# Kernel tuning notes

Measured on AMD Instinct MI355X. Metric: run time of the kernel, lower is better.

The kernel has to match this reference:

```python
import jax, jax.numpy as jnp
import numpy as np

SLIDING_WINDOW = 512  # matches init kwarg
BLOCK_STRIDE = 32     # tokens per cache page


def setup_inputs() -> dict:
    key = jax.random.key(0)
    k0, k1, k2, k3 = jax.random.split(key, 4)
    B, S, HQ, HKV, D = 2, 2048, 32, 8, 128
    nb = S // BLOCK_STRIDE
    q = jax.random.normal(k0, (B, S, HQ, D), jnp.float32)
    k = jax.random.normal(k1, (B, S, HKV, D), jnp.float32)
    v = jax.random.normal(k2, (B, S, HKV, D), jnp.float32)
    sink = jax.random.normal(k3, (HQ,), jnp.float32)
    cache_state = jnp.zeros((B * nb, 2, HKV, BLOCK_STRIDE, D), jnp.float32)
    seq_block_ids = jnp.arange(B * nb, dtype=jnp.int32).reshape(B, nb)
    return {"q": q, "k": k, "v": v, "cache_state": cache_state,
            "seq_block_ids": seq_block_ids, "sink": sink}


def reference(q, k, v, cache_state, seq_block_ids, sink):
    B, S, HQ, D = q.shape
    HKV = k.shape[2]
    G = HQ // HKV  # GQA group size
    stride = cache_state.shape[3]
    nb = S // stride

    # --- write prefill K/V into the paged cache ---
    # pages laid out [num_pages, k/v, HKV, stride, D]
    k_pg = k.reshape(B, nb, stride, HKV, D).transpose(0, 1, 3, 2, 4).reshape(B * nb, HKV, stride, D)
    v_pg = v.reshape(B, nb, stride, HKV, D).transpose(0, 1, 3, 2, 4).reshape(B * nb, HKV, stride, D)
    ids = seq_block_ids.reshape(-1)
    new_cache = cache_state.at[ids, 0].set(k_pg).at[ids, 1].set(v_pg)

    # --- sliding-window causal attention with sink logits (GQA, no repeat) ---
    scale = 1.0 / np.sqrt(D).astype(np.float32)
    qg = q.reshape(B, S, HKV, G, D)
    # scores: [B, HKV, G, Sq, Sk]
    scores = jnp.einsum('bqhgd,bshd->bhgqs', qg, k) * scale
    i = jnp.arange(S)[:, None]
    j = jnp.arange(S)[None, :]
    allowed = (j <= i) & ((i - j) < SLIDING_WINDOW)  # causal banded mask
    neg = jnp.finfo(scores.dtype).min
    scores = jnp.where(allowed, scores, neg)
    # per-head sink logit appended as extra key column, dropped after softmax
    sink_col = jnp.broadcast_to(sink.reshape(HKV, G)[None, :, :, None, None], (B, HKV, G, S, 1))
    probs = jax.nn.softmax(jnp.concatenate([scores, sink_col], axis=-1), axis=-1)[..., :S]
    out = jnp.einsum('bhgqs,bshd->bqhgd', probs, v).reshape(B, S, HQ, D)
    return out, new_cache
```

## Files before the change

kernel.cpp:

```cpp
#include <hip/hip_runtime.h>
#include <hip/hip_bf16.h>
#include <stdint.h>

#define BB 2
#define SS 2048
#define HQ 32
#define HKV 8
#define DD 128
#define WIN 512

typedef __bf16 bf16x8 __attribute__((ext_vector_type(8)));
typedef float f32x16 __attribute__((ext_vector_type(16)));

__device__ __forceinline__ bf16x8 cvt8(float4 a, float4 b, float s) {
  bf16x8 r;
  r[0] = (__bf16)(a.x * s); r[1] = (__bf16)(a.y * s);
  r[2] = (__bf16)(a.z * s); r[3] = (__bf16)(a.w * s);
  r[4] = (__bf16)(b.x * s); r[5] = (__bf16)(b.y * s);
  r[6] = (__bf16)(b.z * s); r[7] = (__bf16)(b.w * s);
  return r;
}

__device__ __forceinline__ uint32_t pk2(float lo, float hi) {
  uint32_t w;
  asm("v_cvt_pk_bf16_f32 %0, %1, %2" : "=v"(w) : "v"(lo), "v"(hi));
  return w;
}

__device__ __forceinline__ unsigned short bfu(float x) {
  union { __bf16 b; unsigned short u; } c; c.b = (__bf16)x; return c.u;
}

#define SWZ(r) ((((r) ^ ((r) >> 3)) & 7) << 4)

__global__ __launch_bounds__(512, 2) void attn_kernel(
    const float* __restrict__ qg, const float* __restrict__ sinkg,
    float* __restrict__ outg,
    const unsigned short* __restrict__ kbg, const unsigned short* __restrict__ vtg)
{
  const int col = (blockIdx.x & 7) + 8 * ((blockIdx.x >> 3) & 1);
  const int rank = blockIdx.x >> 4;
  const int qtile = rank < 24 ? rank + 8 : 31 - rank;
  const int hkv = col & 7, b = col >> 3;
  const int qb = qtile * 64;
  const int tid = threadIdx.x;
  const int wave = tid >> 6, lane = tid & 63;
  const int c5 = lane & 31, hi = lane >> 5;
  const int hq = (hkv << 2) + (wave >> 1);
  const int qw = qb + (wave & 1) * 32;
  const int qrow = qw + c5;

  __shared__ __align__(16) __bf16 Kl[2][64 * 128];
  __shared__ __align__(16) __bf16 Vt[2][128 * 64];

  const float LOG2E = 1.4426950408889634f;
  const float scale = 0.08838834764831845f * LOG2E;
  const float THR = 12.0f;

  bf16x8 qf[8];
  {
    const float* qp = qg + (((size_t)b * SS + qrow) * HQ + hq) * DD + hi * 8;
    #pragma unroll
    for (int ch = 0; ch < 8; ++ch) {
      float4 a = *(const float4*)(qp + ch * 16);
      float4 a2 = *(const float4*)(qp + ch * 16 + 4);
      qf[ch] = cvt8(a, a2, scale);
    }
  }
  const float sk = sinkg[hq] * LOG2E;

  float mm = -1e30f, ll = 0.f;
  f32x16 acc[4];
  #pragma unroll
  for (int d = 0; d < 4; ++d)
    #pragma unroll
    for (int r = 0; r < 16; ++r) acc[d][r] = 0.f;

  const int t0 = (qb > (WIN - 1) ? (qb - (WIN - 1)) : 0) >> 6;
  const int t1 = (qb + 63) >> 6;

  const char* kcol = (const char*)kbg + (size_t)(b * HKV + hkv) * (SS * DD * 2);
  const char* vcol = (const char*)vtg + (size_t)(b * HKV + hkv) * (SS * DD * 2);
  const int p0 = tid * 32;
  const int kr = p0 >> 8, kx = p0 & 255;
  const int vrw = p0 >> 7, vx = p0 & 127;
  const int kd0 = kr * 256 + (kx ^ SWZ(kr)), kd1 = kr * 256 + ((kx + 16) ^ SWZ(kr));
  const int vd0 = vrw * 128 + (vx ^ SWZ(vrw)), vd1 = vrw * 128 + ((vx + 16) ^ SWZ(vrw));

  uint4 ksA, ksB, vsA, vsB;
  auto issue = [&](int t) {
    const char* kt = kcol + (size_t)t * 16384;
    const char* vt = vcol + (size_t)t * 16384;
    ksA = *(const uint4*)(kt + p0); ksB = *(const uint4*)(kt + p0 + 16);
    vsA = *(const uint4*)(vt + p0); vsB = *(const uint4*)(vt + p0 + 16);
  };
  auto commit = [&](int buf) {
    char* kb_ = (char*)&Kl[buf][0]; char* vb_ = (char*)&Vt[buf][0];
    *(uint4*)(kb_ + kd0) = ksA; *(uint4*)(kb_ + kd1) = ksB;
    *(uint4*)(vb_ + vd0) = vsA; *(uint4*)(vb_ + vd1) = vsB;
  };

  issue(t0);
  commit(0);
  __syncthreads();
  int cur = 0;

  const int swA = SWZ(c5);
  const int swB = swA ^ 0x40;

  for (int t = t0; t <= t1; ++t) {
    if (t < t1) issue(t + 1);
    const int kb = t << 6;

    if (kb <= qw + 31 && kb + 63 >= qw - (WIN - 1)) {
      const char* Ksc = (const char*)&Kl[cur][0];
      const char* Vsc = (const char*)&Vt[cur][0];

      f32x16 s0, s1;
      #pragma unroll
      for (int r = 0; r < 16; ++r) { s0[r] = 0.f; s1[r] = 0.f; }
      __builtin_amdgcn_s_setprio(1);
      #pragma unroll
      for (int ch = 0; ch < 8; ++ch) {
        const int colb = ch * 32 + hi * 16;
        bf16x8 a0 = *(const bf16x8*)(Ksc + c5 * 256 + (colb ^ swA));
        bf16x8 a1 = *(const bf16x8*)(Ksc + (32 + c5) * 256 + (colb ^ swB));
        s0 = __builtin_amdgcn_mfma_f32_32x32x16_bf16(a0, qf[ch], s0, 0, 0, 0);
        s1 = __builtin_amdgcn_mfma_f32_32x32x16_bf16(a1, qf[ch], s1, 0, 0, 0);
      }
      __builtin_amdgcn_s_setprio(0);

      const bool noMask = (kb + 63 <= qw) && (kb >= qw - (WIN - 32));

      if (!noMask) {
        #pragma unroll
        for (int r = 0; r < 16; ++r) {
          const int lr = (r & 3) + 8 * (r >> 2) + 4 * hi;
          const int kv0 = kb + lr, kv1 = kv0 + 32;
          const bool ok0 = (kv0 <= qrow) && (qrow - kv0 < WIN);
          const bool ok1 = (kv1 <= qrow) && (qrow - kv1 < WIN);
          s0[r] = ok0 ? s0[r] : -1e30f;
          s1[r] = ok1 ? s1[r] : -1e30f;
        }
      }
      float tmax = s0[0];
      #pragma unroll
      for (int r = 1; r < 16; ++r) tmax = fmaxf(tmax, s0[r]);
      #pragma unroll
      for (int r = 0; r < 16; ++r) tmax = fmaxf(tmax, s1[r]);
      tmax = fmaxf(tmax, __shfl_xor(tmax, 32));

      const bool resc = __any(tmax > mm + THR);
      const float mnew = resc ? fmaxf(mm, tmax) : mm;
      float tsum = 0.f;
      if (noMask) {
        #pragma unroll
        for (int r = 0; r < 16; ++r) {
          s0[r] = exp2f(s0[r] - mnew); tsum += s0[r];
          s1[r] = exp2f(s1[r] - mnew); tsum += s1[r];
        }
      } else {
        #pragma unroll
        for (int r = 0; r < 16; ++r) {
          s0[r] = (s0[r] > -9e29f) ? exp2f(s0[r] - mnew) : 0.f; tsum += s0[r];
          s1[r] = (s1[r] > -9e29f) ? exp2f(s1[r] - mnew) : 0.f; tsum += s1[r];
        }
      }
      tsum += __shfl_xor(tsum, 32);

      if (resc) {
        const float scl = exp2f(mm - mnew);
        ll = ll * scl + tsum;
        #pragma unroll
        for (int d = 0; d < 4; ++d)
          #pragma unroll
          for (int r = 0; r < 16; ++r) acc[d][r] *= scl;
        mm = mnew;
      } else {
        ll += tsum;
      }

      bf16x8 pb[4];
      #pragma unroll
      for (int kvq = 0; kvq < 4; ++kvq) {
        const int bq = (kvq & 1) * 8;
        float e0, e1, e2, e3, e4, e5, e6, e7;
        if (kvq & 2) {
          e0 = s1[bq+0]; e1 = s1[bq+1]; e2 = s1[bq+2]; e3 = s1[bq+3];
          e4 = s1[bq+4]; e5 = s1[bq+5]; e6 = s1[bq+6]; e7 = s1[bq+7];
        } else {
          e0 = s0[bq+0]; e1 = s0[bq+1]; e2 = s0[bq+2]; e3 = s0[bq+3];
          e4 = s0[bq+4]; e5 = s0[bq+5]; e6 = s0[bq+6]; e7 = s0[bq+7];
        }
        const uint32_t A0 = pk2(e0, e1), A1 = pk2(e2, e3);
        const uint32_t B0 = pk2(e4, e5), B1 = pk2(e6, e7);
        const uint32_t XA0 = __shfl_xor(A0, 32), XA1 = __shfl_xor(A1, 32);
        const uint32_t XB0 = __shfl_xor(B0, 32), XB1 = __shfl_xor(B1, 32);
        union { uint4 u; bf16x8 v; } cvu;
        cvu.u.x = hi ? XB0 : A0;
        cvu.u.y = hi ? XB1 : A1;
        cvu.u.z = hi ? B0 : XA0;
        cvu.u.w = hi ? B1 : XA1;
        pb[kvq] = cvu.v;
      }

      __builtin_amdgcn_s_setprio(1);
      #pragma unroll
      for (int d = 0; d < 4; ++d) {
        const int rowb = (d * 32 + c5) * 128;
        const int swV = swA ^ ((d & 1) << 6);
        #pragma unroll
        for (int kvq = 0; kvq < 4; ++kvq) {
          bf16x8 va = *(const bf16x8*)(Vsc + rowb + ((kvq * 32 + hi * 16) ^ swV));
          acc[d] = __builtin_amdgcn_mfma_f32_32x32x16_bf16(va, pb[kvq], acc[d], 0, 0, 0);
        }
      }
      __builtin_amdgcn_s_setprio(0);
    }

    if (t < t1) {
      commit(cur ^ 1);
      __syncthreads();
      cur ^= 1;
    }
  }

  {
    const float Mf = fmaxf(mm, sk);
    const float ex = exp2f(mm - Mf);
    const float denom = ll * ex + exp2f(sk - Mf);
    const float fac = ex / denom;
    float* orow = outg + (((size_t)b * SS + qrow) * HQ + hq) * DD;
    #pragma unroll
    for (int d = 0; d < 4; ++d) {
      #pragma unroll
      for (int q4 = 0; q4 < 4; ++q4) {
        float4 o;
        o.x = acc[d][q4 * 4 + 0] * fac;
        o.y = acc[d][q4 * 4 + 1] * fac;
        o.z = acc[d][q4 * 4 + 2] * fac;
        o.w = acc[d][q4 * 4 + 3] * fac;
        *(float4*)(orow + d * 32 + q4 * 8 + 4 * hi) = o;
      }
    }
  }
}

__global__ void prep_kv(const float* __restrict__ kg, const float* __restrict__ vg,
                        unsigned short* __restrict__ kb, unsigned short* __restrict__ vt) {
  const int bx = blockIdx.x;
  const int t = bx & 31, colx = bx >> 5;
  const int b = colx >> 3, hkv = colx & 7;
  const int kbrow = t * 64;
  if (blockIdx.y == 0) {
    #pragma unroll
    for (int i = 0; i < 8; ++i) {
      const int idx = i * 1024 + threadIdx.x * 4;
      const int r = idx >> 7, d = idx & 127;
      float4 v = *(const float4*)(kg + (((size_t)b * SS + kbrow + r) * HKV + hkv) * DD + d);
      ushort4 o = make_ushort4(bfu(v.x), bfu(v.y), bfu(v.z), bfu(v.w));
      *(ushort4*)(kb + ((size_t)colx * SS + kbrow + r) * DD + d) = o;
    }
  } else {
    __shared__ unsigned short Vl[64][132];
    #pragma unroll
    for (int i = 0; i < 8; ++i) {
      const int idx = i * 1024 + threadIdx.x * 4;
      const int kv = idx >> 7, d = idx & 127;
      float4 v = *(const float4*)(vg + (((size_t)b * SS + kbrow + kv) * HKV + hkv) * DD + d);
      Vl[kv][d + 0] = bfu(v.x); Vl[kv][d + 1] = bfu(v.y);
      Vl[kv][d + 2] = bfu(v.z); Vl[kv][d + 3] = bfu(v.w);
    }
    __syncthreads();
    #pragma unroll
    for (int i = 0; i < 8; ++i) {
      const int idx = i * 1024 + threadIdx.x * 4;
      const int d = idx >> 6, kv = idx & 63;
      ushort4 o = make_ushort4(Vl[kv + 0][d], Vl[kv + 1][d], Vl[kv + 2][d], Vl[kv + 3][d]);
      *(ushort4*)(vt + ((size_t)colx * 32 + t) * 8192 + d * 64 + kv) = o;
    }
  }
}

__global__ __launch_bounds__(512, 2) void attn_fallback(
    const float* __restrict__ qg, const float* __restrict__ kg,
    const float* __restrict__ vg, const float* __restrict__ sinkg,
    float* __restrict__ outg)
{
  const int col = (blockIdx.x & 7) + 8 * ((blockIdx.x >> 3) & 1);
  const int rank = blockIdx.x >> 4;
  const int qtile = rank < 24 ? rank + 8 : 31 - rank;
  const int hkv = col & 7, b = col >> 3;
  const int qb = qtile * 64;
  const int tid = threadIdx.x;
  const int wave = tid >> 6, lane = tid & 63;
  const int c5 = lane & 31, hi = lane >> 5;
  const int hq = (hkv << 2) + (wave >> 1);
  const int qw = qb + (wave & 1) * 32;
  const int qrow = qw + c5;

  __shared__ __align__(16) __bf16 Kl[2][64 * 128];
  __shared__ __align__(16) __bf16 Vt[2][128 * 64];

  const float LOG2E = 1.4426950408889634f;
  const float scale = 0.08838834764831845f * LOG2E;
  const float THR = 12.0f;

  bf16x8 qf[8];
  {
    const float* qp = qg + (((size_t)b * SS + qrow) * HQ + hq) * DD + hi * 8;
    #pragma unroll
    for (int ch = 0; ch < 8; ++ch) {
      float4 a = *(const float4*)(qp + ch * 16);
      float4 a2 = *(const float4*)(qp + ch * 16 + 4);
      qf[ch] = cvt8(a, a2, scale);
    }
  }
  const float sk = sinkg[hq] * LOG2E;

  float mm = -1e30f, ll = 0.f;
  f32x16 acc[4];
  #pragma unroll
  for (int d = 0; d < 4; ++d)
    #pragma unroll
    for (int r = 0; r < 16; ++r) acc[d][r] = 0.f;

  const int t0 = (qb > (WIN - 1) ? (qb - (WIN - 1)) : 0) >> 6;
  const int t1 = (qb + 63) >> 6;

  const int krow = tid >> 3, kchunk = tid & 7;
  const int vd = tid & 127, vslot = tid >> 7;
  const size_t KSTEP = (size_t)64 * HKV * DD;
  const float* kBase = kg + (((size_t)b * SS + krow) * HKV + hkv) * DD + kchunk * 16;
  const float* vBase = vg + (((size_t)b * SS + vslot * 16) * HKV + hkv) * DD + vd;

  float4 k0, k1, k2, k3; float vr[16];
  auto issue = [&](int t) {
    const float* kp = kBase + (size_t)t * KSTEP;
    k0 = *(const float4*)(kp);     k1 = *(const float4*)(kp + 4);
    k2 = *(const float4*)(kp + 8); k3 = *(const float4*)(kp + 12);
    const float* vp = vBase + (size_t)t * KSTEP;
    #pragma unroll
    for (int j = 0; j < 16; ++j) vr[j] = vp[(size_t)j * (HKV * DD)];
  };
  const int ksw = SWZ(krow);
  const int vsw = SWZ(vd);
  auto commit = [&](int buf) {
    char* kd = (char*)(&Kl[buf][0]) + krow * 256;
    *(bf16x8*)(kd + ((kchunk * 32) ^ ksw)) = cvt8(k0, k1, 1.f);
    *(bf16x8*)(kd + ((kchunk * 32 + 16) ^ ksw)) = cvt8(k2, k3, 1.f);
    char* vdst = (char*)(&Vt[buf][0]) + vd * 128;
    bf16x8 w0, w1;
    #pragma unroll
    for (int j = 0; j < 8; ++j) { w0[j] = (__bf16)vr[j]; w1[j] = (__bf16)vr[8 + j]; }
    *(bf16x8*)(vdst + ((vslot * 32) ^ vsw)) = w0;
    *(bf16x8*)(vdst + ((vslot * 32 + 16) ^ vsw)) = w1;
  };

  issue(t0);
  commit(0);
  __syncthreads();
  int cur = 0;

  const int swA = SWZ(c5);
  const int swB = swA ^ 0x40;

  for (int t = t0; t <= t1; ++t) {
    if (t < t1) issue(t + 1);
    const int kb = t << 6;
    if (kb <= qw + 31 && kb + 63 >= qw - (WIN - 1)) {
      const char* Ksc = (const char*)&Kl[cur][0];
      const char* Vsc = (const char*)&Vt[cur][0];
      f32x16 s0, s1;
      #pragma unroll
      for (int r = 0; r < 16; ++r) { s0[r] = 0.f; s1[r] = 0.f; }
      __builtin_amdgcn_s_setprio(1);
      #pragma unroll
      for (int ch = 0; ch < 8; ++ch) {
        const int colb = ch * 32 + hi * 16;
        bf16x8 a0 = *(const bf16x8*)(Ksc + c5 * 256 + (colb ^ swA));
        bf16x8 a1 = *(const bf16x8*)(Ksc + (32 + c5) * 256 + (colb ^ swB));
        s0 = __builtin_amdgcn_mfma_f32_32x32x16_bf16(a0, qf[ch], s0, 0, 0, 0);
        s1 = __builtin_amdgcn_mfma_f32_32x32x16_bf16(a1, qf[ch], s1, 0, 0, 0);
      }
      __builtin_amdgcn_s_setprio(0);

      const bool noMask = (kb + 63 <= qw) && (kb >= qw - (WIN - 32));
      if (!noMask) {
        #pragma unroll
        for (int r = 0; r < 16; ++r) {
          const int lr = (r & 3) + 8 * (r >> 2) + 4 * hi;
          const int kv0 = kb + lr, kv1 = kv0 + 32;
          const bool ok0 = (kv0 <= qrow) && (qrow - kv0 < WIN);
          const bool ok1 = (kv1 <= qrow) && (qrow - kv1 < WIN);
          s0[r] = ok0 ? s0[r] : -1e30f;
          s1[r] = ok1 ? s1[r] : -1e30f;
        }
      }
      float tmax = s0[0];
      #pragma unroll
      for (int r = 1; r < 16; ++r) tmax = fmaxf(tmax, s0[r]);
      #pragma unroll
      for (int r = 0; r < 16; ++r) tmax = fmaxf(tmax, s1[r]);
      tmax = fmaxf(tmax, __shfl_xor(tmax, 32));
      const bool resc = __any(tmax > mm + THR);
      const float mnew = resc ? fmaxf(mm, tmax) : mm;
      float tsum = 0.f;
      if (noMask) {
        #pragma unroll
        for (int r = 0; r < 16; ++r) {
          s0[r] = exp2f(s0[r] - mnew); tsum += s0[r];
          s1[r] = exp2f(s1[r] - mnew); tsum += s1[r];
        }
      } else {
        #pragma unroll
        for (int r = 0; r < 16; ++r) {
          s0[r] = (s0[r] > -9e29f) ? exp2f(s0[r] - mnew) : 0.f; tsum += s0[r];
          s1[r] = (s1[r] > -9e29f) ? exp2f(s1[r] - mnew) : 0.f; tsum += s1[r];
        }
      }
      tsum += __shfl_xor(tsum, 32);
      if (resc) {
        const float scl = exp2f(mm - mnew);
        ll = ll * scl + tsum;
        #pragma unroll
        for (int d = 0; d < 4; ++d)
          #pragma unroll
          for (int r = 0; r < 16; ++r) acc[d][r] *= scl;
        mm = mnew;
      } else {
        ll += tsum;
      }
      bf16x8 pb[4];
      #pragma unroll
      for (int kvq = 0; kvq < 4; ++kvq) {
        const int bq = (kvq & 1) * 8;
        float e0, e1, e2, e3, e4, e5, e6, e7;
        if (kvq & 2) {
          e0 = s1[bq+0]; e1 = s1[bq+1]; e2 = s1[bq+2]; e3 = s1[bq+3];
          e4 = s1[bq+4]; e5 = s1[bq+5]; e6 = s1[bq+6]; e7 = s1[bq+7];
        } else {
          e0 = s0[bq+0]; e1 = s0[bq+1]; e2 = s0[bq+2]; e3 = s0[bq+3];
          e4 = s0[bq+4]; e5 = s0[bq+5]; e6 = s0[bq+6]; e7 = s0[bq+7];
        }
        const uint32_t A0 = pk2(e0, e1), A1 = pk2(e2, e3);
        const uint32_t B0 = pk2(e4, e5), B1 = pk2(e6, e7);
        const uint32_t XA0 = __shfl_xor(A0, 32), XA1 = __shfl_xor(A1, 32);
        const uint32_t XB0 = __shfl_xor(B0, 32), XB1 = __shfl_xor(B1, 32);
        union { uint4 u; bf16x8 v; } cvu;
        cvu.u.x = hi ? XB0 : A0;
        cvu.u.y = hi ? XB1 : A1;
        cvu.u.z = hi ? B0 : XA0;
        cvu.u.w = hi ? B1 : XA1;
        pb[kvq] = cvu.v;
      }
      __builtin_amdgcn_s_setprio(1);
      #pragma unroll
      for (int d = 0; d < 4; ++d) {
        const int rowb = (d * 32 + c5) * 128;
        const int swV = swA ^ ((d & 1) << 6);
        #pragma unroll
        for (int kvq = 0; kvq < 4; ++kvq) {
          bf16x8 va = *(const bf16x8*)(Vsc + rowb + ((kvq * 32 + hi * 16) ^ swV));
          acc[d] = __builtin_amdgcn_mfma_f32_32x32x16_bf16(va, pb[kvq], acc[d], 0, 0, 0);
        }
      }
      __builtin_amdgcn_s_setprio(0);
    }
    if (t < t1) {
      commit(cur ^ 1);
      __syncthreads();
      cur ^= 1;
    }
  }
  {
    const float Mf = fmaxf(mm, sk);
    const float ex = exp2f(mm - Mf);
    const float denom = ll * ex + exp2f(sk - Mf);
    const float fac = ex / denom;
    float* orow = outg + (((size_t)b * SS + qrow) * HQ + hq) * DD;
    #pragma unroll
    for (int d = 0; d < 4; ++d) {
      #pragma unroll
      for (int q4 = 0; q4 < 4; ++q4) {
        float4 o;
        o.x = acc[d][q4 * 4 + 0] * fac;
        o.y = acc[d][q4 * 4 + 1] * fac;
        o.z = acc[d][q4 * 4 + 2] * fac;
        o.w = acc[d][q4 * 4 + 3] * fac;
        *(float4*)(orow + d * 32 + q4 * 8 + 4 * hi) = o;
      }
    }
  }
}

__global__ void build_inv(const int* __restrict__ ids, int* __restrict__ inv,
                          int npages, int nslots) {
  const int i = threadIdx.x;
  if (i < npages) inv[i] = -1;
  __syncthreads();
  if (i < nslots) inv[ids[i]] = i;
}

__global__ void page_fill(const float* __restrict__ kg, const float* __restrict__ vg,
                          const float* __restrict__ cache_in, const int* __restrict__ inv,
                          float* __restrict__ cache) {
  const int page = blockIdx.x, half = blockIdx.y;
  const int slot = inv[page];
  float4* d4 = (float4*)cache;
  const size_t dbase = (((size_t)page * 2 + half) * 8) * 1024;
  if (slot >= 0) {
    const int b = slot >> 6, blk = slot & 63;
    const float4* s4 = (const float4*)(half ? vg : kg);
    for (int f = threadIdx.x; f < 8192; f += blockDim.x) {
      const int d = f & 31, s = (f >> 5) & 31, h = f >> 10;
      d4[dbase + (size_t)h * 1024 + s * 32 + d] =
          s4[(((size_t)b * SS + blk * 32 + s) * 8 + h) * 32 + d];
    }
  } else {
    const float4* s4 = (const float4*)cache_in;
    for (int f = threadIdx.x; f < 8192; f += blockDim.x)
      d4[dbase + f] = s4[dbase + f];
  }
}

__global__ void cache_copy(const float* __restrict__ src, float* __restrict__ dst, int n4) {
  const float4* s = (const float4*)src;
  float4* d = (float4*)dst;
  for (int i = blockIdx.x * blockDim.x + threadIdx.x; i < n4; i += gridDim.x * blockDim.x)
    d[i] = s[i];
}
__global__ void cache_scatter(const float* __restrict__ kg, const float* __restrict__ vg,
                              const int* __restrict__ ids, float* __restrict__ cache) {
  const int slot = blockIdx.x;
  const int half = blockIdx.y;
  const int b = slot >> 6, blk = slot & 63;
  const int page = ids[slot];
  const float4* s4 = (const float4*)(half ? vg : kg);
  float4* d4 = (float4*)cache;
  for (int f = threadIdx.x; f < 8192; f += blockDim.x) {
    const int d = f & 31, s = (f >> 5) & 31, h = f >> 10;
    d4[(((size_t)page * 2 + half) * 8 + h) * 1024 + s * 32 + d] =
        s4[(((size_t)b * SS + blk * 32 + s) * 8 + h) * 32 + d];
  }
}

extern "C" void kernel_launch(void* const* d_in, const int* in_sizes, int n_in,
                              void* d_out, int out_size, void* d_ws, size_t ws_size,
                              hipStream_t stream) {
  const float* q = (const float*)d_in[0];
  const float* k = (const float*)d_in[1];
  const float* v = (const float*)d_in[2];
  const float* cache_in = (const float*)d_in[3];
  const int* ids = (const int*)d_in[4];
  const float* sink = (const float*)d_in[5];
  float* out = (float*)d_out;
  float* cache_out = out + (size_t)BB * SS * HQ * DD;

  const int nslots = in_sizes[4];
  const int npages = in_sizes[3] / (2 * HKV * 32 * DD);

  const size_t kvBytes = (size_t)BB * HKV * SS * DD * 2;
  const size_t need = 4096 + 2 * kvBytes;
  const bool smallMaps = (npages <= 1024) && (nslots <= 1024);

  if (ws_size >= need && smallMaps) {
    int* inv = (int*)d_ws;
    unsigned short* kbp = (unsigned short*)((char*)d_ws + 4096);
    unsigned short* vtp = kbp + kvBytes / 2;
    build_inv<<<1, 1024, 0, stream>>>(ids, inv, npages, nslots);
    page_fill<<<dim3(npages, 2), 256, 0, stream>>>(k, v, cache_in, inv, cache_out);
    prep_kv<<<dim3(BB * HKV * 32, 2), 256, 0, stream>>>(k, v, kbp, vtp);
    attn_kernel<<<512, 512, 0, stream>>>(q, sink, out, kbp, vtp);
  } else if (ws_size >= (size_t)npages * sizeof(int) && smallMaps) {
    int* inv = (int*)d_ws;
    build_inv<<<1, 1024, 0, stream>>>(ids, inv, npages, nslots);
    page_fill<<<dim3(npages, 2), 256, 0, stream>>>(k, v, cache_in, inv, cache_out);
    attn_fallback<<<512, 512, 0, stream>>>(q, k, v, sink, out);
  } else {
    cache_copy<<<4096, 256, 0, stream>>>(cache_in, cache_out, (BB * SS * HKV * DD * 2) / 4);
    cache_scatter<<<dim3(BB * 64, 2), 256, 0, stream>>>(k, v, ids, cache_out);
    attn_fallback<<<512, 512, 0, stream>>>(q, k, v, sink, out);
  }
}
```

Before: 107.8 us.

## Pre-swizzle K/V tiles and stage them with direct global-to-LDS loads

prep_kv now writes a combined K/V image per head column in which each 64-token tile is already in the swizzled LDS layout. The attention kernel copies these tiles into shared memory with global_load_lds, removing the register round-trip and manual commit stores. Blocks now cover 128 query rows for two query heads, and the block-to-work mapping is reordered so more K/V reuse happens per block. The fallback kernel also loses its setprio hints and its unmasked exp fast path. This relies on the image layout matching the in-kernel swizzle exactly, and the larger tiles change the load balance across blocks.

```diff
diff --git a/kernel.cpp b/kernel.cpp
--- a/kernel.cpp
+++ b/kernel.cpp
@@ -11,6 +11,13 @@
 
 typedef __bf16 bf16x8 __attribute__((ext_vector_type(8)));
 typedef float f32x16 __attribute__((ext_vector_type(16)));
+typedef unsigned int u32;
+typedef __attribute__((address_space(3))) u32 lds_u32;
+typedef const __attribute__((address_space(1))) u32 glb_u32;
+
+__device__ __forceinline__ void gld_lds16(const void* g, void* l) {
+  __builtin_amdgcn_global_load_lds((glb_u32*)g, (lds_u32*)l, 16, 0, 0);
+}
 
 __device__ __forceinline__ bf16x8 cvt8(float4 a, float4 b, float s) {
   bf16x8 r;
@@ -35,23 +42,24 @@
 
 __global__ __launch_bounds__(512, 2) void attn_kernel(
     const float* __restrict__ qg, const float* __restrict__ sinkg,
-    float* __restrict__ outg,
-    const unsigned short* __restrict__ kbg, const unsigned short* __restrict__ vtg)
+    float* __restrict__ outg, const char* __restrict__ kvimg)
 {
-  const int col = (blockIdx.x & 7) + 8 * ((blockIdx.x >> 3) & 1);
-  const int rank = blockIdx.x >> 4;
-  const int qtile = rank < 24 ? rank + 8 : 31 - rank;
+  const int sid = (blockIdx.x & 7) * 64 + (blockIdx.x >> 3);
+  const int col = sid >> 5;
+  const int r = sid & 31;
+  const int hp = r & 1;
+  const int qtile = 15 - (r >> 1);
   const int hkv = col & 7, b = col >> 3;
-  const int qb = qtile * 64;
+  const int qb = qtile * 128;
   const int tid = threadIdx.x;
   const int wave = tid >> 6, lane = tid & 63;
   const int c5 = lane & 31, hi = lane >> 5;
-  const int hq = (hkv << 2) + (wave >> 1);
-  const int qw = qb + (wave & 1) * 32;
+  const int wq = wave & 3, wh = wave >> 2;
+  const int hq = (hkv << 2) + hp * 2 + wh;
+  const int qw = qb + wq * 32;
   const int qrow = qw + c5;
 
-  __shared__ __align__(16) __bf16 Kl[2][64 * 128];
-  __shared__ __align__(16) __bf16 Vt[2][128 * 64];
+  __shared__ __align__(16) char Buf[2][32768];
 
   const float LOG2E = 1.4426950408889634f;
   const float scale = 0.08838834764831845f * LOG2E;
@@ -74,34 +82,21 @@
   #pragma unroll
   for (int d = 0; d < 4; ++d)
     #pragma unroll
-    for (int r = 0; r < 16; ++r) acc[d][r] = 0.f;
-
-  const int t0 = (qb > (WIN - 1) ? (qb - (WIN - 1)) : 0) >> 6;
-  const int t1 = (qb + 63) >> 6;
-
-  const char* kcol = (const char*)kbg + (size_t)(b * HKV + hkv) * (SS * DD * 2);
-  const char* vcol = (const char*)vtg + (size_t)(b * HKV + hkv) * (SS * DD * 2);
-  const int p0 = tid * 32;
-  const int kr = p0 >> 8, kx = p0 & 255;
-  const int vrw = p0 >> 7, vx = p0 & 127;
-  const int kd0 = kr * 256 + (kx ^ SWZ(kr)), kd1 = kr * 256 + ((kx + 16) ^ SWZ(kr));
-  const int vd0 = vrw * 128 + (vx ^ SWZ(vrw)), vd1 = vrw * 128 + ((vx + 16) ^ SWZ(vrw));
-
-  uint4 ksA, ksB, vsA, vsB;
-  auto issue = [&](int t) {
-    const char* kt = kcol + (size_t)t * 16384;
-    const char* vt = vcol + (size_t)t * 16384;
-    ksA = *(const uint4*)(kt + p0); ksB = *(const uint4*)(kt + p0 + 16);
-    vsA = *(const uint4*)(vt + p0); vsB = *(const uint4*)(vt + p0 + 16);
+    for (int r2 = 0; r2 < 16; ++r2) acc[d][r2] = 0.f;
+
+  const int t0 = (qb > 511 ? (qb - 511) >> 6 : 0);
+  const int t1 = (qb + 127) >> 6;
+
+  const char* colbase = kvimg + (size_t)col * (32 * 32768);
+  auto stage = [&](int t, int buf) {
+    const char* src = colbase + (size_t)t * 32768 + wave * 4096 + lane * 16;
+    char* dst = &Buf[buf][wave * 4096];
+    #pragma unroll
+    for (int i = 0; i < 4; ++i)
+      gld_lds16(src + i * 1024, dst + i * 1024);
   };
-  auto commit = [&](int buf) {
-    char* kb_ = (char*)&Kl[buf][0]; char* vb_ = (char*)&Vt[buf][0];
-    *(uint4*)(kb_ + kd0) = ksA; *(uint4*)(kb_ + kd1) = ksB;
-    *(uint4*)(vb_ + vd0) = vsA; *(uint4*)(vb_ + vd1) = vsB;
-  };
-
-  issue(t0);
-  commit(0);
+
+  stage(t0, 0);
   __syncthreads();
   int cur = 0;
 
@@ -109,16 +104,16 @@
   const int swB = swA ^ 0x40;
 
   for (int t = t0; t <= t1; ++t) {
-    if (t < t1) issue(t + 1);
+    if (t < t1) stage(t + 1, cur ^ 1);
     const int kb = t << 6;
 
     if (kb <= qw + 31 && kb + 63 >= qw - (WIN - 1)) {
-      const char* Ksc = (const char*)&Kl[cur][0];
-      const char* Vsc = (const char*)&Vt[cur][0];
+      const char* Ksc = &Buf[cur][0];
+      const char* Vsc = &Buf[cur][16384];
 
       f32x16 s0, s1;
       #pragma unroll
-      for (int r = 0; r < 16; ++r) { s0[r] = 0.f; s1[r] = 0.f; }
+      for (int r2 = 0; r2 < 16; ++r2) { s0[r2] = 0.f; s1[r2] = 0.f; }
       __builtin_amdgcn_s_setprio(1);
       #pragma unroll
       for (int ch = 0; ch < 8; ++ch) {
@@ -134,20 +129,20 @@
 
       if (!noMask) {
         #pragma unroll
-        for (int r = 0; r < 16; ++r) {
-          const int lr = (r & 3) + 8 * (r >> 2) + 4 * hi;
+        for (int r2 = 0; r2 < 16; ++r2) {
+          const int lr = (r2 & 3) + 8 * (r2 >> 2) + 4 * hi;
           const int kv0 = kb + lr, kv1 = kv0 + 32;
           const bool ok0 = (kv0 <= qrow) && (qrow - kv0 < WIN);
           const bool ok1 = (kv1 <= qrow) && (qrow - kv1 < WIN);
-          s0[r] = ok0 ? s0[r] : -1e30f;
-          s1[r] = ok1 ? s1[r] : -1e30f;
+          s0[r2] = ok0 ? s0[r2] : -1e30f;
+          s1[r2] = ok1 ? s1[r2] : -1e30f;
         }
       }
       float tmax = s0[0];
       #pragma unroll
-      for (int r = 1; r < 16; ++r) tmax = fmaxf(tmax, s0[r]);
-      #pragma unroll
-      for (int r = 0; r < 16; ++r) tmax = fmaxf(tmax, s1[r]);
+      for (int r2 = 1; r2 < 16; ++r2) tmax = fmaxf(tmax, s0[r2]);
+      #pragma unroll
+      for (int r2 = 0; r2 < 16; ++r2) tmax = fmaxf(tmax, s1[r2]);
       tmax = fmaxf(tmax, __shfl_xor(tmax, 32));
 
       const bool resc = __any(tmax > mm + THR);
@@ -155,15 +150,15 @@
       float tsum = 0.f;
       if (noMask) {
         #pragma unroll
-        for (int r = 0; r < 16; ++r) {
-          s0[r] = exp2f(s0[r] - mnew); tsum += s0[r];
-          s1[r] = exp2f(s1[r] - mnew); tsum += s1[r];
+        for (int r2 = 0; r2 < 16; ++r2) {
+          s0[r2] = exp2f(s0[r2] - mnew); tsum += s0[r2];
+          s1[r2] = exp2f(s1[r2] - mnew); tsum += s1[r2];
         }
       } else {
         #pragma unroll
-        for (int r = 0; r < 16; ++r) {
-          s0[r] = (s0[r] > -9e29f) ? exp2f(s0[r] - mnew) : 0.f; tsum += s0[r];
-          s1[r] = (s1[r] > -9e29f) ? exp2f(s1[r] - mnew) : 0.f; tsum += s1[r];
+        for (int r2 = 0; r2 < 16; ++r2) {
+          s0[r2] = (s0[r2] > -9e29f) ? exp2f(s0[r2] - mnew) : 0.f; tsum += s0[r2];
+          s1[r2] = (s1[r2] > -9e29f) ? exp2f(s1[r2] - mnew) : 0.f; tsum += s1[r2];
         }
       }
       tsum += __shfl_xor(tsum, 32);
@@ -174,7 +169,7 @@
         #pragma unroll
         for (int d = 0; d < 4; ++d)
           #pragma unroll
-          for (int r = 0; r < 16; ++r) acc[d][r] *= scl;
+          for (int r2 = 0; r2 < 16; ++r2) acc[d][r2] *= scl;
         mm = mnew;
       } else {
         ll += tsum;
@@ -219,7 +214,6 @@
     }
 
     if (t < t1) {
-      commit(cur ^ 1);
       __syncthreads();
       cur ^= 1;
     }
@@ -247,37 +241,41 @@
 }
 
 __global__ void prep_kv(const float* __restrict__ kg, const float* __restrict__ vg,
-                        unsigned short* __restrict__ kb, unsigned short* __restrict__ vt) {
-  const int bx = blockIdx.x;
-  const int t = bx & 31, colx = bx >> 5;
+                        char* __restrict__ kvimg) {
+  const int t = blockIdx.x & 31, colx = blockIdx.x >> 5;
   const int b = colx >> 3, hkv = colx & 7;
-  const int kbrow = t * 64;
+  const int kb = t * 64;
+  unsigned short* img = (unsigned short*)(kvimg + (size_t)colx * (32 * 32768) + (size_t)t * 32768);
   if (blockIdx.y == 0) {
     #pragma unroll
     for (int i = 0; i < 8; ++i) {
-      const int idx = i * 1024 + threadIdx.x * 4;
-      const int r = idx >> 7, d = idx & 127;
-      float4 v = *(const float4*)(kg + (((size_t)b * SS + kbrow + r) * HKV + hkv) * DD + d);
-      ushort4 o = make_ushort4(bfu(v.x), bfu(v.y), bfu(v.z), bfu(v.w));
-      *(ushort4*)(kb + ((size_t)colx * SS + kbrow + r) * DD + d) = o;
+      const int c = i * 256 + threadIdx.x;
+      const int kr = c >> 5, j0 = (c & 31) * 4;
+      const int kx = ((kr ^ (kr >> 3)) & 7) << 3;
+      const float* sp = kg + (((size_t)b * SS + kb + kr) * HKV + hkv) * DD + (j0 ^ kx);
+      float4 a = *(const float4*)sp;
+      *(ushort4*)(img + kr * 128 + j0) = make_ushort4(bfu(a.x), bfu(a.y), bfu(a.z), bfu(a.w));
     }
   } else {
+    unsigned short* vimg = img + 8192;
     __shared__ unsigned short Vl[64][132];
     #pragma unroll
     for (int i = 0; i < 8; ++i) {
       const int idx = i * 1024 + threadIdx.x * 4;
       const int kv = idx >> 7, d = idx & 127;
-      float4 v = *(const float4*)(vg + (((size_t)b * SS + kbrow + kv) * HKV + hkv) * DD + d);
+      float4 v = *(const float4*)(vg + (((size_t)b * SS + kb + kv) * HKV + hkv) * DD + d);
       Vl[kv][d + 0] = bfu(v.x); Vl[kv][d + 1] = bfu(v.y);
       Vl[kv][d + 2] = bfu(v.z); Vl[kv][d + 3] = bfu(v.w);
     }
     __syncthreads();
     #pragma unroll
     for (int i = 0; i < 8; ++i) {
-      const int idx = i * 1024 + threadIdx.x * 4;
-      const int d = idx >> 6, kv = idx & 63;
-      ushort4 o = make_ushort4(Vl[kv + 0][d], Vl[kv + 1][d], Vl[kv + 2][d], Vl[kv + 3][d]);
-      *(ushort4*)(vt + ((size_t)colx * 32 + t) * 8192 + d * 64 + kv) = o;
+      const int c = i * 256 + threadIdx.x;
+      const int vd = c >> 4, j0 = (c & 15) * 4;
+      const int vx = ((vd ^ (vd >> 3)) & 7) << 3;
+      const int js = j0 ^ vx;
+      *(ushort4*)(vimg + vd * 64 + j0) =
+          make_ushort4(Vl[js + 0][vd], Vl[js + 1][vd], Vl[js + 2][vd], Vl[js + 3][vd]);
     }
   }
 }
@@ -374,7 +372,6 @@
       f32x16 s0, s1;
       #pragma unroll
       for (int r = 0; r < 16; ++r) { s0[r] = 0.f; s1[r] = 0.f; }
-      __builtin_amdgcn_s_setprio(1);
       #pragma unroll
       for (int ch = 0; ch < 8; ++ch) {
         const int colb = ch * 32 + hi * 16;
@@ -383,8 +380,6 @@
         s0 = __builtin_amdgcn_mfma_f32_32x32x16_bf16(a0, qf[ch], s0, 0, 0, 0);
         s1 = __builtin_amdgcn_mfma_f32_32x32x16_bf16(a1, qf[ch], s1, 0, 0, 0);
       }
-      __builtin_amdgcn_s_setprio(0);
-
       const bool noMask = (kb + 63 <= qw) && (kb >= qw - (WIN - 32));
       if (!noMask) {
         #pragma unroll
@@ -406,18 +401,10 @@
       const bool resc = __any(tmax > mm + THR);
       const float mnew = resc ? fmaxf(mm, tmax) : mm;
       float tsum = 0.f;
-      if (noMask) {
-        #pragma unroll
-        for (int r = 0; r < 16; ++r) {
-          s0[r] = exp2f(s0[r] - mnew); tsum += s0[r];
-          s1[r] = exp2f(s1[r] - mnew); tsum += s1[r];
-        }
-      } else {
-        #pragma unroll
-        for (int r = 0; r < 16; ++r) {
-          s0[r] = (s0[r] > -9e29f) ? exp2f(s0[r] - mnew) : 0.f; tsum += s0[r];
-          s1[r] = (s1[r] > -9e29f) ? exp2f(s1[r] - mnew) : 0.f; tsum += s1[r];
-        }
+      #pragma unroll
+      for (int r = 0; r < 16; ++r) {
+        s0[r] = (s0[r] > -9e29f) ? exp2f(s0[r] - mnew) : 0.f; tsum += s0[r];
+        s1[r] = (s1[r] > -9e29f) ? exp2f(s1[r] - mnew) : 0.f; tsum += s1[r];
       }
       tsum += __shfl_xor(tsum, 32);
       if (resc) {
@@ -454,7 +441,6 @@
         cvu.u.w = hi ? B1 : XA1;
         pb[kvq] = cvu.v;
       }
-      __builtin_amdgcn_s_setprio(1);
       #pragma unroll
       for (int d = 0; d < 4; ++d) {
         const int rowb = (d * 32 + c5) * 128;
@@ -465,7 +451,6 @@
           acc[d] = __builtin_amdgcn_mfma_f32_32x32x16_bf16(va, pb[kvq], acc[d], 0, 0, 0);
         }
       }
-      __builtin_amdgcn_s_setprio(0);
     }
     if (t < t1) {
       commit(cur ^ 1);
@@ -560,18 +545,17 @@
   const int nslots = in_sizes[4];
   const int npages = in_sizes[3] / (2 * HKV * 32 * DD);
 
-  const size_t kvBytes = (size_t)BB * HKV * SS * DD * 2;
-  const size_t need = 4096 + 2 * kvBytes;
+  const size_t imgBytes = (size_t)16 * 32 * 32768;
+  const size_t need = 4096 + imgBytes;
   const bool smallMaps = (npages <= 1024) && (nslots <= 1024);
 
   if (ws_size >= need && smallMaps) {
     int* inv = (int*)d_ws;
-    unsigned short* kbp = (unsigned short*)((char*)d_ws + 4096);
-    unsigned short* vtp = kbp + kvBytes / 2;
+    char* kvimg = (char*)d_ws + 4096;
     build_inv<<<1, 1024, 0, stream>>>(ids, inv, npages, nslots);
     page_fill<<<dim3(npages, 2), 256, 0, stream>>>(k, v, cache_in, inv, cache_out);
-    prep_kv<<<dim3(BB * HKV * 32, 2), 256, 0, stream>>>(k, v, kbp, vtp);
-    attn_kernel<<<512, 512, 0, stream>>>(q, sink, out, kbp, vtp);
+    prep_kv<<<dim3(16 * 32, 2), 256, 0, stream>>>(k, v, kvimg);
+    attn_kernel<<<512, 512, 0, stream>>>(q, sink, out, kvimg);
   } else if (ws_size >= (size_t)npages * sizeof(int) && smallMaps) {
     int* inv = (int*)d_ws;
     build_inv<<<1, 1024, 0, stream>>>(ids, inv, npages, nslots);
```

Result: no change. 107.4 us (-0.4%).
